# Kernel tuning notes

Hardware: AMD Instinct MI355X
Metric: run time of the kernel (lower is better)

Reference implementation:

```python
import jax, jax.numpy as jnp
import numpy as np
import math

N = 50000   # nodes
E = 800000  # edges
D = 128     # in/out dim
T = 4       # node types
H = 8       # heads (forced: Linear(8,64).view(-1, H, 8))
DK = D // H
HD = 8      # h_mat feature dim


def setup_inputs() -> dict:
    key = jax.random.key(0)
    ks = jax.random.split(key, 16)
    g = lambda k, shp, fan: jax.random.uniform(k, shp, jnp.float32, -1.0, 1.0) * math.sqrt(6.0 / fan)
    return {
        "meta_xs": jax.random.normal(ks[0], (N, D), jnp.float32),
        "node_type": jax.random.randint(ks[1], (N,), 0, T),
        "edge_index": jax.random.randint(ks[2], (2, E), 0, N),
        "h_mat": jax.random.normal(ks[3], (N, HD), jnp.float32),
        "sub_W": g(ks[4], (T, D, D), 2 * D),
        "sub_b": jnp.zeros((T, D), jnp.float32),
        "neigh_W": g(ks[5], (T, D, D), 2 * D),
        "neigh_b": jnp.zeros((T, D), jnp.float32),
        "hsub_W": g(ks[6], (HD, H * HD), HD + H * HD),
        "hsub_b": jnp.zeros((H * HD,), jnp.float32),
        "hneigh_W": g(ks[7], (HD, H * HD), HD + H * HD),
        "hneigh_b": jnp.zeros((H * HD,), jnp.float32),
        "relation_att": g(ks[8], (T, H, DK), H + DK),
        "relation_h_att": g(ks[9], (T, H, HD), H + HD),
        "ln_gamma": jnp.ones((D,), jnp.float32),
        "ln_beta": jnp.zeros((D,), jnp.float32),
    }


def _hgt_forward(meta_xs, h_mat, sub_W, sub_b, neigh_W, neigh_b, hsub_W, hsub_b,
                 hneigh_W, hneigh_b, relation_att, relation_h_att, ln_gamma, ln_beta,
                 node_type, edge_index):
    n = meta_xs.shape[0]
    e = edge_index.shape[1]
    src = edge_index[0]  # edge_index_j (neighbor)
    dst = edge_index[1]  # edge_index_i (sub / target)
    sqrt_dk = math.sqrt(DK)
    d_h = math.sqrt(H)

    # per-node, type-selected linear projections (sub by own type, neigh by own type)
    q_all = jnp.einsum('nd,tdo->tno', meta_xs, sub_W) + sub_b[:, None, :]      # [T,N,D]
    k_all = jnp.einsum('nd,tdo->tno', meta_xs, neigh_W) + neigh_b[:, None, :]  # [T,N,D]
    ar = jnp.arange(n)
    q_node = q_all[node_type, ar]  # [N,D] sub_linear[type_i](x_i)
    k_node = k_all[node_type, ar]  # [N,D] neigh_linear[type_j](x_j)

    h_sub_node = (h_mat @ hsub_W + hsub_b).reshape(n, H, HD)
    h_neigh_node = (h_mat @ hneigh_W + hneigh_b).reshape(n, H, HD)

    st = node_type[dst]  # sub type per edge selects relation params
    h_s = h_sub_node[dst]    # [E,H,8]
    h_n = h_neigh_node[src]  # [E,H,8]
    att_h = jnp.sum(jnp.tanh(h_s * h_n) * relation_h_att[st], axis=-1) / d_h  # [E,H]

    q_e = q_node[dst].reshape(e, H, DK)
    k_e = k_node[src].reshape(e, H, DK)
    att = jnp.sum(jnp.tanh(q_e * k_e) * relation_att[st], axis=-1) / sqrt_dk * att_h  # [E,H]

    # edge softmax over destination segments
    m = jax.ops.segment_max(att, dst, num_segments=n)  # [N,H]
    ea = jnp.exp(att - m[dst])
    denom = jax.ops.segment_sum(ea, dst, num_segments=n)
    alpha = ea / (denom[dst] + 1e-16)  # [E,H]

    msg = (k_e * alpha[:, :, None]).reshape(e, D)
    aggr = jax.ops.segment_sum(msg, dst, num_segments=n)  # [N,D]

    out = jax.nn.gelu(aggr, approximate=False)
    mu = jnp.mean(out, axis=-1, keepdims=True)
    var = jnp.var(out, axis=-1, keepdims=True)
    return (out - mu) * jax.lax.rsqrt(var + 1e-5) * ln_gamma + ln_beta


def reference(meta_xs, node_type, edge_index, h_mat, sub_W, sub_b, neigh_W, neigh_b,
              hsub_W, hsub_b, hneigh_W, hneigh_b, relation_att, relation_h_att,
              ln_gamma, ln_beta):
    return _hgt_forward(meta_xs, h_mat, sub_W, sub_b, neigh_W, neigh_b, hsub_W, hsub_b,
                        hneigh_W, hneigh_b, relation_att, relation_h_att, ln_gamma, ln_beta,
                        node_type, edge_index)
```

## Files before the change

kernel.cpp:

```cpp
#include <hip/hip_runtime.h>

typedef __bf16 bf16x8 __attribute__((ext_vector_type(8)));
typedef float f32x4 __attribute__((ext_vector_type(4)));

#define B_CHUNK 64
#define R_RANGE 4

__device__ __forceinline__ float exp2_fast(float x){
#if __has_builtin(__builtin_amdgcn_exp2f)
  return __builtin_amdgcn_exp2f(x);
#else
  return __expf(x * 0.69314718055994531f);
#endif
}
template<int CTRL>
__device__ __forceinline__ float dpp_add(float x){
  union { float f; int i; } a, b;
  a.f = x;
  b.i = __builtin_amdgcn_mov_dpp(a.i, CTRL, 0xF, 0xF, true);
  return x + b.f;
}
__device__ __forceinline__ float sum4(float x){
  x = dpp_add<0xB1>(x);
  x = dpp_add<0x4E>(x);
  return x;
}
__device__ __forceinline__ unsigned int cvt_pk_bf16(float lo, float hi){
  unsigned int r;
  asm("v_cvt_pk_bf16_f32 %0, %1, %2" : "=v"(r) : "v"(lo), "v"(hi));
  return r;
}
__device__ __forceinline__ unsigned short f2bf1(float f){
  return (unsigned short)cvt_pk_bf16(f, f);
}
__device__ __forceinline__ bf16x8 ld_bf8(const unsigned short* p){
  union { uint4 u; bf16x8 v; } c;
  c.u = *reinterpret_cast<const uint4*>(p);
  return c.v;
}
__device__ __forceinline__ bf16x8 ld_f32_to_bf8(const float* p){
  float4 lo = *reinterpret_cast<const float4*>(p);
  float4 hi = *reinterpret_cast<const float4*>(p + 4);
  union { unsigned int u[4]; bf16x8 v; } c;
  c.u[0] = cvt_pk_bf16(lo.x, lo.y);
  c.u[1] = cvt_pk_bf16(lo.z, lo.w);
  c.u[2] = cvt_pk_bf16(hi.x, hi.y);
  c.u[3] = cvt_pk_bf16(hi.z, hi.w);
  return c.v;
}

__global__ __launch_bounds__(256) void k_prep(const int* ntype, int* tcur, int* nbt,
                       int Npad, int N,
                       const float* subW, const float* neighW,
                       unsigned short* wts, unsigned short* wtn,
                       const int* ei, int E, unsigned short* hist,
                       int RNG, int HR, int NB, int WB){
  __shared__ unsigned int lsh[6272];
  int b = blockIdx.x;
  if (b < NB){
    int i = b*256 + threadIdx.x;
    if (i >= N) return;
    int lane = threadIdx.x & 63;
    int myt = ntype[i];
    unsigned long long below = (lane == 0) ? 0ull : ((~0ull) >> (64 - lane));
    #pragma unroll
    for (int tt = 0; tt < 4; ++tt){
      unsigned long long mask = __ballot(myt == tt);
      if (mask){
        int leader = __ffsll((long long)mask) - 1;
        int base = 0;
        if (lane == leader) base = atomicAdd(&tcur[tt], __popcll(mask));
        base = __shfl(base, leader);
        if (myt == tt){
          int pos = base + __popcll(mask & below);
          nbt[tt*Npad + pos] = i;
        }
      }
    }
  } else if (b < NB + WB){
    int i = (b - NB)*256 + threadIdx.x;
    int w = i >> 16;
    int r = i & 65535;
    int t = r >> 14;
    int rem = r & 16383;
    int o = rem >> 7;
    int kd = rem & 127;
    const float* src = w ? neighW : subW;
    unsigned short* dstp = w ? wtn : wts;
    dstp[(t << 14) + (o << 7) + kd] = f2bf1(src[(t << 14) + (kd << 7) + o]);
  } else {
    int sb = b - NB - WB;
    int cb = sb & (B_CHUNK - 1);
    int r  = sb / B_CHUNK;
    int lo = r * RNG;
    int half = RNG >> 1;
    for (int i = threadIdx.x; i < half; i += 256) lsh[i] = 0;
    __syncthreads();
    int C = (E + B_CHUNK - 1) / B_CHUNK;
    int e0 = cb * C;
    int e1 = e0 + C; if (e1 > E) e1 = E;
    for (int i = e0 + threadIdx.x; i < e1; i += 256){
      int d = ei[E + i] - lo;
      if ((unsigned)d < (unsigned)RNG)
        atomicAdd(&lsh[d >> 1], (d & 1) ? 65536u : 1u);
    }
    __syncthreads();
    unsigned int* hrow = reinterpret_cast<unsigned int*>(hist + (size_t)cb*HR + lo);
    for (int i = threadIdx.x; i < half; i += 256) hrow[i] = lsh[i];
  }
}

__global__ __launch_bounds__(256) void k_scan(unsigned short* hist, int HR,
                                              int* deg, int N){
  int d = blockIdx.x*256 + threadIdx.x;
  if (d >= N) return;
  unsigned run = 0;
  #pragma unroll 4
  for (int b = 0; b < B_CHUNK; ++b){
    unsigned short* p = hist + (size_t)b*HR + d;
    unsigned v = *p;
    *p = (unsigned short)run;
    run += v;
  }
  deg[d] = (int)run;
}

__global__ __launch_bounds__(256) void k_mix(const float* X,
      const unsigned short* wts, const unsigned short* wtn,
      const float* sub_b, const float* neigh_b,
      const int* nbt, const int* tcur, int Npad,
      float* q, char* kkc,
      const int* ei, unsigned short* bucket, int E,
      unsigned short* hist, int RNG, int HR,
      const float* h_mat, const float* hsW, const float* hsb,
      const float* hnW, const float* hnb,
      float2* hs2, char* hnc, int N, int MB, int SBL){
  __shared__ unsigned int lsh[6272];
  int b = blockIdx.x;
  if (b < MB){
    int t = -1, chunk = 0, acc = 0;
    #pragma unroll
    for (int tt = 0; tt < 4; ++tt){
      int cnt = tcur[tt];
      int nc = (cnt + 63) >> 6;
      if (t < 0 && b < acc + nc){ t = tt; chunk = b - acc; }
      acc += nc;
    }
    if (t < 0) return;
    int lane = threadIdx.x & 63;
    int w = threadIdx.x >> 6;
    int quad = lane >> 4, l16 = lane & 15;
    int cnt = tcur[t];
    int p = chunk*64 + w*16 + l16;
    bool ok = p < cnt;
    int nid = nbt[t*Npad + (ok ? p : 0)];
    bf16x8 xb[4];
    #pragma unroll
    for (int kk = 0; kk < 4; ++kk)
      xb[kk] = ld_f32_to_bf8(X + (size_t)nid*128 + kk*32 + quad*8);
    #pragma unroll
    for (int pj = 0; pj < 2; ++pj){
      const unsigned short* Wt = pj ? wtn : wts;
      const float* bias = pj ? neigh_b : sub_b;
      #pragma unroll
      for (int ot = 0; ot < 8; ++ot){
        f32x4 c = {0.f, 0.f, 0.f, 0.f};
        #pragma unroll
        for (int kk = 0; kk < 4; ++kk){
          bf16x8 wa = ld_bf8(Wt + ((size_t)t << 14) + ((size_t)(ot*16 + l16) << 7)
                                + kk*32 + quad*8);
          c = __builtin_amdgcn_mfma_f32_16x16x32_bf16(wa, xb[kk], c, 0, 0, 0);
        }
        int o0 = ot*16 + quad*4;
        float4 b4 = *reinterpret_cast<const float4*>(bias + t*128 + o0);
        if (ok){
          if (pj == 0){
            float4 v = make_float4(c[0]+b4.x, c[1]+b4.y, c[2]+b4.z, c[3]+b4.w);
            *reinterpret_cast<float4*>(q + (size_t)nid*128 + o0) = v;
          } else {
            uint2 pk;
            pk.x = cvt_pk_bf16(c[0]+b4.x, c[1]+b4.y);
            pk.y = cvt_pk_bf16(c[2]+b4.z, c[3]+b4.w);
            *reinterpret_cast<uint2*>(kkc + ((size_t)nid << 8) + (size_t)(o0 << 1)) = pk;
          }
        }
      }
    }
  } else if (b < MB + SBL){
    int sb = b - MB;
    int cb = sb & (B_CHUNK - 1);
    int r  = sb / B_CHUNK;
    int lo = r * RNG;
    int half = RNG >> 1;
    const unsigned int* hrow =
        reinterpret_cast<const unsigned int*>(hist + (size_t)cb*HR + lo);
    for (int i = threadIdx.x; i < half; i += 256) lsh[i] = hrow[i];
    __syncthreads();
    int C = (E + B_CHUNK - 1) / B_CHUNK;
    int e0 = cb * C;
    int e1 = e0 + C; if (e1 > E) e1 = E;
    for (int i = e0 + threadIdx.x; i < e1; i += 256){
      int d = ei[E + i];
      int rb = d - lo;
      if ((unsigned)rb < (unsigned)RNG){
        unsigned old = atomicAdd(&lsh[rb >> 1], (rb & 1) ? 65536u : 1u);
        unsigned pos = (old >> ((rb & 1) << 4)) & 0xffffu;
        if (pos < 128)
          bucket[(size_t)d*128 + pos] = (unsigned short)ei[i];
      }
    }
  } else {
    int i = (b - MB - SBL)*256 + threadIdx.x;
    if (i >= N*32) return;
    int n = i >> 5, l = i & 31;
    const float* hm = h_mat + (size_t)n*8;
    const float2* hsW2 = reinterpret_cast<const float2*>(hsW);
    const float2* hnW2 = reinterpret_cast<const float2*>(hnW);
    float s0=0.f, s1=0.f, n0=0.f, n1=0.f;
    #pragma unroll
    for (int d = 0; d < 8; ++d){
      float hv = hm[d];
      float2 ws2 = hsW2[d*32 + l];
      float2 wn2 = hnW2[d*32 + l];
      s0 += hv * ws2.x; s1 += hv * ws2.y;
      n0 += hv * wn2.x; n1 += hv * wn2.y;
    }
    float2 bs = reinterpret_cast<const float2*>(hsb)[l];
    float2 bn = reinterpret_cast<const float2*>(hnb)[l];
    hs2[(size_t)i] = make_float2(s0 + bs.x, s1 + bs.y);
    *reinterpret_cast<unsigned int*>(hnc + (size_t)n*128 + l*4)
        = cvt_pk_bf16(n0 + bn.x, n1 + bn.y);
  }
}

__global__ __launch_bounds__(256) void k_edge(const float* q, const char* kkc,
      const char* hnc, const float2* hs2, const int* degA,
      const unsigned short* bucket, const int* ntype,
      const float* rel_att, const float* rel_h_att,
      const float* ln_g, const float* ln_b,
      float* out, int N){
  int wid = (blockIdx.x*blockDim.x + threadIdx.x) >> 6;
  if (wid >= N) return;
  int lane = threadIdx.x & 63;
  int l = lane & 31;
  int half = (lane >> 5) & 1;
  int t4 = l & 3, head = l >> 2;
  const float TLOG2E = 2.8853900817779268f;
  float4 qv = *reinterpret_cast<const float4*>(q + (size_t)wid*128 + l*4);
  float qe0 = qv.x*TLOG2E, qe1 = qv.y*TLOG2E, qe2 = qv.z*TLOG2E, qe3 = qv.w*TLOG2E;
  float2 hv = hs2[(size_t)wid*32 + l];
  float he0 = hv.x*TLOG2E, he1 = hv.y*TLOG2E;
  int st = ntype[wid];
  int rb = st*8 + head;
  float4 ra = *reinterpret_cast<const float4*>(rel_att + rb*16 + t4*4);
  float2 rh = *reinterpret_cast<const float2*>(rel_h_att + rb*8 + t4*2);
  float c0 = -0.5f*ra.x, c1 = -0.5f*ra.y, c2 = -0.5f*ra.z, c3 = -0.5f*ra.w;
  float cs = 0.25f*(ra.x + ra.y + ra.z + ra.w);
  const float HSC = 0.35355339059327373f * 1.4426950408889634f;
  float rh0 = rh.x*HSC, rh1 = rh.y*HSC;
  float ch0 = -2.f*rh0, ch1 = -2.f*rh1, chs = rh0 + rh1;
  float s = 0.f, a0 = 0.f, a1 = 0.f, a2 = 0.f, a3 = 0.f;

  int deg = __builtin_amdgcn_readfirstlane(degA[wid]);
  if (deg > 128) deg = 128;
  unsigned bkt = reinterpret_cast<const unsigned*>(bucket)[(size_t)wid*64 + lane];
  int niter = (deg + 1) >> 1;
  const char* kk_l = kkc + l*8;
  const char* hn_l = hnc + l*4;

  struct KH { uint2 k; unsigned h; };
  auto lp = [&](int g)->KH {
    int gg = g < niter ? g : 0;
    unsigned v = (unsigned)__builtin_amdgcn_readlane((int)bkt, gg);
    int sA = (int)(v & 0xffffu);
    int sB = (2*gg + 1 < deg) ? (int)(v >> 16) : sA;
    int sy = half ? sB : sA;
    KH r;
    r.k = *reinterpret_cast<const uint2*>(kk_l + ((size_t)(unsigned)sy << 8));
    r.h = *reinterpret_cast<const unsigned*>(hn_l + ((size_t)(unsigned)sy << 7));
    return r;
  };
  auto pr = [&](KH P, int g){
    union { unsigned u; float f; } k0,k1,k2,k3,h0,h1;
    k0.u = P.k.x << 16; k1.u = P.k.x & 0xffff0000u;
    k2.u = P.k.y << 16; k3.u = P.k.y & 0xffff0000u;
    h0.u = P.h << 16;   h1.u = P.h & 0xffff0000u;
    float e0 = exp2_fast(qe0*k0.f), e1 = exp2_fast(qe1*k1.f);
    float e2 = exp2_fast(qe2*k2.f), e3 = exp2_fast(qe3*k3.f);
    float f0 = exp2_fast(he0*h0.f), f1 = exp2_fast(he1*h1.f);
    float r0 = __builtin_amdgcn_rcpf(e0 + 1.f), r1 = __builtin_amdgcn_rcpf(e1 + 1.f);
    float r2 = __builtin_amdgcn_rcpf(e2 + 1.f), r3 = __builtin_amdgcn_rcpf(e3 + 1.f);
    float g0 = __builtin_amdgcn_rcpf(f0 + 1.f), g1 = __builtin_amdgcn_rcpf(f1 + 1.f);
    float pp = fmaf(c0,r0, fmaf(c1,r1, fmaf(c2,r2, fmaf(c3,r3, cs))));
    float ph = fmaf(ch0,g0, fmaf(ch1,g1, chs));
    pp = sum4(pp);
    ph = sum4(ph);
    float w = exp2_fast(pp * ph);
    w = (2*g + half < deg) ? w : 0.f;
    s += w;
    a0 = fmaf(w, k0.f, a0); a1 = fmaf(w, k1.f, a1);
    a2 = fmaf(w, k2.f, a2); a3 = fmaf(w, k3.f, a3);
  };

  if (niter > 0){
    KH A = lp(0);
    KH B = lp(1);
    for (int g = 0; g < niter; g += 2){
      KH C = lp(g+2);
      pr(A, g);
      KH D = lp(g+3);
      if (g+1 < niter) pr(B, g+1);
      A = C; B = D;
    }
  }
  s  += __shfl_xor(s, 32);
  a0 += __shfl_xor(a0, 32); a1 += __shfl_xor(a1, 32);
  a2 += __shfl_xor(a2, 32); a3 += __shfl_xor(a3, 32);

  float inv = 1.0f / (s + 1e-16f);
  float x0 = a0*inv, x1 = a1*inv, x2 = a2*inv, x3 = a3*inv;
  const float IS2 = 0.70710678118654752f;
  x0 = 0.5f*x0*(1.f + erff(x0*IS2));
  x1 = 0.5f*x1*(1.f + erff(x1*IS2));
  x2 = 0.5f*x2*(1.f + erff(x2*IS2));
  x3 = 0.5f*x3*(1.f + erff(x3*IS2));
  float sm = x0+x1+x2+x3;
  float sq = x0*x0 + x1*x1 + x2*x2 + x3*x3;
  #pragma unroll
  for (int d = 1; d < 32; d <<= 1){ sm += __shfl_xor(sm, d); sq += __shfl_xor(sq, d); }
  float mu = sm * (1.f/128.f);
  float var = fmaxf(sq * (1.f/128.f) - mu*mu, 0.f);
  float r = rsqrtf(var + 1e-5f);
  if (half == 0){
    float4 g4 = *reinterpret_cast<const float4*>(ln_g + l*4);
    float4 b4 = *reinterpret_cast<const float4*>(ln_b + l*4);
    float4 o4 = make_float4((x0-mu)*r*g4.x + b4.x, (x1-mu)*r*g4.y + b4.y,
                            (x2-mu)*r*g4.z + b4.z, (x3-mu)*r*g4.w + b4.w);
    *reinterpret_cast<float4*>(out + (size_t)wid*128 + l*4) = o4;
  }
}

extern "C" void kernel_launch(void* const* d_in, const int* in_sizes, int n_in,
                              void* d_out, int out_size, void* d_ws, size_t ws_size,
                              hipStream_t stream) {
  const float* meta_xs  = (const float*)d_in[0];
  const int*   node_type= (const int*)d_in[1];
  const int*   edge_idx = (const int*)d_in[2];
  const float* h_mat    = (const float*)d_in[3];
  const float* sub_W    = (const float*)d_in[4];
  const float* sub_b    = (const float*)d_in[5];
  const float* neigh_W  = (const float*)d_in[6];
  const float* neigh_b  = (const float*)d_in[7];
  const float* hsub_W   = (const float*)d_in[8];
  const float* hsub_b   = (const float*)d_in[9];
  const float* hneigh_W = (const float*)d_in[10];
  const float* hneigh_b = (const float*)d_in[11];
  const float* rel_att  = (const float*)d_in[12];
  const float* rel_hatt = (const float*)d_in[13];
  const float* ln_g     = (const float*)d_in[14];
  const float* ln_b     = (const float*)d_in[15];

  const int N = in_sizes[0] / 128;
  const int E = in_sizes[2] / 2;
  const int Npad = (N + 63) & ~63;
  const int RNG = (((N + R_RANGE - 1) / R_RANGE) + 1) & ~1;
  const int HR  = RNG * R_RANGE;

  char* wbase = (char*)d_ws;
  size_t o = 0;
  auto carve = [&](size_t bytes)->char* {
    char* p = wbase + o;
    o = (o + bytes + 255) & ~(size_t)255;
    return p;
  };
  float*          q      = (float*)carve((size_t)N*128*4);
  char*           kkc    = carve((size_t)N*256);
  char*           hnc    = carve((size_t)N*128);
  float2*         hs2    = (float2*)carve((size_t)N*32*8);
  unsigned short* bucket = (unsigned short*)carve((size_t)N*128*2);
  unsigned short* hist   = (unsigned short*)carve((size_t)B_CHUNK*HR*2);
  int*            deg    = (int*)carve((size_t)N*4);
  int*            tmeta  = (int*)carve(64);
  int*            nbt    = (int*)carve((size_t)4*Npad*4);
  unsigned short* wts    = (unsigned short*)carve((size_t)4*128*128*2);
  unsigned short* wtn    = (unsigned short*)carve((size_t)4*128*128*2);
  if (o > ws_size) return;

  int* tcur = tmeta;

  const int NB  = (N + 255) / 256;
  const int WB  = (2*4*128*128) / 256;
  const int SBL = B_CHUNK * R_RANGE;
  const int MB  = ((N + 63) >> 6) + 4;
  const int HB  = (N*32 + 255) / 256;

  hipMemsetAsync(tmeta, 0, 64, stream);
  k_prep <<<NB + WB + SBL, 256, 0, stream>>>(node_type, tcur, nbt, Npad, N,
                                       sub_W, neigh_W, wts, wtn,
                                       edge_idx, E, hist, RNG, HR, NB, WB);
  k_scan <<<(N + 255)/256, 256, 0, stream>>>(hist, HR, deg, N);
  k_mix  <<<MB + SBL + HB, 256, 0, stream>>>(meta_xs, wts, wtn, sub_b, neigh_b,
                                       nbt, tcur, Npad, q, kkc,
                                       edge_idx, bucket, E, hist, RNG, HR,
                                       h_mat, hsub_W, hsub_b, hneigh_W, hneigh_b,
                                       hs2, hnc, N, MB, SBL);
  k_edge <<<(N+3)/4, 256, 0, stream>>>(q, kkc, hnc, hs2, deg, bucket, node_type,
                                       rel_att, rel_hatt, ln_g, ln_b,
                                       (float*)d_out, N);
}
```

Before: 292.5 us.

## Record per-edge ranks during histogram pass to make scatter atomic-free

The histogram pass now stores each edge's local rank within its (chunk, destination) bin. The bucket scatter then becomes a plain lookup of prefix plus rank with no shared-memory atomics, and it is split into finer per-chunk segments for more parallelism. The destination range split is halved, so each histogram block covers twice as many bins and uses more LDS, and the h_mat projections move next to the scan kernel. This adds a per-edge rank buffer write and read in exchange for removing the repeated range filtering and the second round of atomics in the scatter.

```diff
diff --git a/kernel.cpp b/kernel.cpp
--- a/kernel.cpp
+++ b/kernel.cpp
@@ -4,7 +4,7 @@
 typedef float f32x4 __attribute__((ext_vector_type(4)));
 
 #define B_CHUNK 64
-#define R_RANGE 4
+#define R_RANGE 2
 
 __device__ __forceinline__ float exp2_fast(float x){
 #if __has_builtin(__builtin_amdgcn_exp2f)
@@ -54,11 +54,32 @@
                        const float* subW, const float* neighW,
                        unsigned short* wts, unsigned short* wtn,
                        const int* ei, int E, unsigned short* hist,
-                       int RNG, int HR, int NB, int WB){
-  __shared__ unsigned int lsh[6272];
+                       unsigned short* rank, int RNG, int HR, int NB){
+  __shared__ unsigned int lsh[12544];
   int b = blockIdx.x;
-  if (b < NB){
-    int i = b*256 + threadIdx.x;
+  const int SB1 = B_CHUNK * R_RANGE;
+  if (b < SB1){
+    int cb = b & (B_CHUNK - 1);
+    int r  = b >> 6;
+    int lo = r * RNG;
+    int bins = RNG >> 1;
+    for (int i = threadIdx.x; i < bins; i += 256) lsh[i] = 0;
+    __syncthreads();
+    int C = (E + B_CHUNK - 1) / B_CHUNK;
+    int e0 = cb * C;
+    int e1 = e0 + C; if (e1 > E) e1 = E;
+    for (int i = e0 + threadIdx.x; i < e1; i += 256){
+      int d = ei[E + i] - lo;
+      if ((unsigned)d < (unsigned)RNG){
+        unsigned old = atomicAdd(&lsh[d >> 1], (d & 1) ? 65536u : 1u);
+        rank[i] = (unsigned short)((old >> ((d & 1) << 4)) & 0xffffu);
+      }
+    }
+    __syncthreads();
+    unsigned int* hrow = reinterpret_cast<unsigned int*>(hist + (size_t)cb*HR + lo);
+    for (int i = threadIdx.x; i < bins; i += 256) hrow[i] = lsh[i];
+  } else if (b < SB1 + NB){
+    int i = (b - SB1)*256 + threadIdx.x;
     if (i >= N) return;
     int lane = threadIdx.x & 63;
     int myt = ntype[i];
@@ -77,8 +98,8 @@
         }
       }
     }
-  } else if (b < NB + WB){
-    int i = (b - NB)*256 + threadIdx.x;
+  } else {
+    int i = (b - SB1 - NB)*256 + threadIdx.x;
     int w = i >> 16;
     int r = i & 65535;
     int t = r >> 14;
@@ -88,54 +109,58 @@
     const float* src = w ? neighW : subW;
     unsigned short* dstp = w ? wtn : wts;
     dstp[(t << 14) + (o << 7) + kd] = f2bf1(src[(t << 14) + (kd << 7) + o]);
+  }
+}
+
+__global__ __launch_bounds__(256) void k_mid(unsigned short* hist, int HR,
+                       int* deg, int N, int SCB,
+                       const float* h_mat, const float* hsW, const float* hsb,
+                       const float* hnW, const float* hnb,
+                       float2* hs2, char* hnc){
+  int b = blockIdx.x;
+  if (b < SCB){
+    int d = b*256 + threadIdx.x;
+    if (d >= N) return;
+    unsigned run = 0;
+    #pragma unroll 4
+    for (int c = 0; c < B_CHUNK; ++c){
+      unsigned short* p = hist + (size_t)c*HR + d;
+      unsigned v = *p;
+      *p = (unsigned short)run;
+      run += v;
+    }
+    deg[d] = (int)run;
   } else {
-    int sb = b - NB - WB;
-    int cb = sb & (B_CHUNK - 1);
-    int r  = sb / B_CHUNK;
-    int lo = r * RNG;
-    int half = RNG >> 1;
-    for (int i = threadIdx.x; i < half; i += 256) lsh[i] = 0;
-    __syncthreads();
-    int C = (E + B_CHUNK - 1) / B_CHUNK;
-    int e0 = cb * C;
-    int e1 = e0 + C; if (e1 > E) e1 = E;
-    for (int i = e0 + threadIdx.x; i < e1; i += 256){
-      int d = ei[E + i] - lo;
-      if ((unsigned)d < (unsigned)RNG)
-        atomicAdd(&lsh[d >> 1], (d & 1) ? 65536u : 1u);
-    }
-    __syncthreads();
-    unsigned int* hrow = reinterpret_cast<unsigned int*>(hist + (size_t)cb*HR + lo);
-    for (int i = threadIdx.x; i < half; i += 256) hrow[i] = lsh[i];
+    int i = (b - SCB)*256 + threadIdx.x;
+    if (i >= N*32) return;
+    int n = i >> 5, l = i & 31;
+    const float* hm = h_mat + (size_t)n*8;
+    const float2* hsW2 = reinterpret_cast<const float2*>(hsW);
+    const float2* hnW2 = reinterpret_cast<const float2*>(hnW);
+    float s0=0.f, s1=0.f, n0=0.f, n1=0.f;
+    #pragma unroll
+    for (int d = 0; d < 8; ++d){
+      float hv = hm[d];
+      float2 ws2 = hsW2[d*32 + l];
+      float2 wn2 = hnW2[d*32 + l];
+      s0 += hv * ws2.x; s1 += hv * ws2.y;
+      n0 += hv * wn2.x; n1 += hv * wn2.y;
+    }
+    float2 bs = reinterpret_cast<const float2*>(hsb)[l];
+    float2 bn = reinterpret_cast<const float2*>(hnb)[l];
+    hs2[(size_t)i] = make_float2(s0 + bs.x, s1 + bs.y);
+    *reinterpret_cast<unsigned int*>(hnc + (size_t)n*128 + l*4)
+        = cvt_pk_bf16(n0 + bn.x, n1 + bn.y);
   }
 }
 
-__global__ __launch_bounds__(256) void k_scan(unsigned short* hist, int HR,
-                                              int* deg, int N){
-  int d = blockIdx.x*256 + threadIdx.x;
-  if (d >= N) return;
-  unsigned run = 0;
-  #pragma unroll 4
-  for (int b = 0; b < B_CHUNK; ++b){
-    unsigned short* p = hist + (size_t)b*HR + d;
-    unsigned v = *p;
-    *p = (unsigned short)run;
-    run += v;
-  }
-  deg[d] = (int)run;
-}
-
-__global__ __launch_bounds__(256) void k_mix(const float* X,
+__global__ __launch_bounds__(256) void k_ms(const float* X,
       const unsigned short* wts, const unsigned short* wtn,
       const float* sub_b, const float* neigh_b,
       const int* nbt, const int* tcur, int Npad,
       float* q, char* kkc,
       const int* ei, unsigned short* bucket, int E,
-      unsigned short* hist, int RNG, int HR,
-      const float* h_mat, const float* hsW, const float* hsb,
-      const float* hnW, const float* hnb,
-      float2* hs2, char* hnc, int N, int MB, int SBL){
-  __shared__ unsigned int lsh[6272];
+      const unsigned short* hist, int HR, const unsigned short* rank, int MB){
   int b = blockIdx.x;
   if (b < MB){
     int t = -1, chunk = 0, acc = 0;
@@ -186,50 +211,22 @@
         }
       }
     }
-  } else if (b < MB + SBL){
+  } else {
     int sb = b - MB;
-    int cb = sb & (B_CHUNK - 1);
-    int r  = sb / B_CHUNK;
-    int lo = r * RNG;
-    int half = RNG >> 1;
-    const unsigned int* hrow =
-        reinterpret_cast<const unsigned int*>(hist + (size_t)cb*HR + lo);
-    for (int i = threadIdx.x; i < half; i += 256) lsh[i] = hrow[i];
-    __syncthreads();
+    int cb = sb >> 3;
+    int sub = sb & 7;
     int C = (E + B_CHUNK - 1) / B_CHUNK;
-    int e0 = cb * C;
-    int e1 = e0 + C; if (e1 > E) e1 = E;
+    int seg = (C + 7) >> 3;
+    int s0 = sub*seg;
+    int s1 = s0 + seg; if (s1 > C) s1 = C;
+    int e0 = cb*C + s0;
+    int e1 = cb*C + s1; if (e1 > E) e1 = E;
+    const unsigned short* hrow = hist + (size_t)cb*HR;
     for (int i = e0 + threadIdx.x; i < e1; i += 256){
       int d = ei[E + i];
-      int rb = d - lo;
-      if ((unsigned)rb < (unsigned)RNG){
-        unsigned old = atomicAdd(&lsh[rb >> 1], (rb & 1) ? 65536u : 1u);
-        unsigned pos = (old >> ((rb & 1) << 4)) & 0xffffu;
-        if (pos < 128)
-          bucket[(size_t)d*128 + pos] = (unsigned short)ei[i];
-      }
-    }
-  } else {
-    int i = (b - MB - SBL)*256 + threadIdx.x;
-    if (i >= N*32) return;
-    int n = i >> 5, l = i & 31;
-    const float* hm = h_mat + (size_t)n*8;
-    const float2* hsW2 = reinterpret_cast<const float2*>(hsW);
-    const float2* hnW2 = reinterpret_cast<const float2*>(hnW);
-    float s0=0.f, s1=0.f, n0=0.f, n1=0.f;
-    #pragma unroll
-    for (int d = 0; d < 8; ++d){
-      float hv = hm[d];
-      float2 ws2 = hsW2[d*32 + l];
-      float2 wn2 = hnW2[d*32 + l];
-      s0 += hv * ws2.x; s1 += hv * ws2.y;
-      n0 += hv * wn2.x; n1 += hv * wn2.y;
-    }
-    float2 bs = reinterpret_cast<const float2*>(hsb)[l];
-    float2 bn = reinterpret_cast<const float2*>(hnb)[l];
-    hs2[(size_t)i] = make_float2(s0 + bs.x, s1 + bs.y);
-    *reinterpret_cast<unsigned int*>(hnc + (size_t)n*128 + l*4)
-        = cvt_pk_bf16(n0 + bn.x, n1 + bn.y);
+      int pos = (int)hrow[d] + (int)rank[i];
+      if (pos < 128) bucket[(size_t)d*128 + pos] = (unsigned short)ei[i];
+    }
   }
 }
 
@@ -379,6 +376,7 @@
   float2*         hs2    = (float2*)carve((size_t)N*32*8);
   unsigned short* bucket = (unsigned short*)carve((size_t)N*128*2);
   unsigned short* hist   = (unsigned short*)carve((size_t)B_CHUNK*HR*2);
+  unsigned short* rank   = (unsigned short*)carve((size_t)E*2);
   int*            deg    = (int*)carve((size_t)N*4);
   int*            tmeta  = (int*)carve(64);
   int*            nbt    = (int*)carve((size_t)4*Npad*4);
@@ -388,22 +386,24 @@
 
   int* tcur = tmeta;
 
+  const int SB1 = B_CHUNK * R_RANGE;
   const int NB  = (N + 255) / 256;
   const int WB  = (2*4*128*128) / 256;
-  const int SBL = B_CHUNK * R_RANGE;
+  const int SCB = (N + 255) / 256;
+  const int HB  = (N*32 + 255) / 256;
   const int MB  = ((N + 63) >> 6) + 4;
-  const int HB  = (N*32 + 255) / 256;
+  const int SB3 = B_CHUNK * 8;
 
   hipMemsetAsync(tmeta, 0, 64, stream);
-  k_prep <<<NB + WB + SBL, 256, 0, stream>>>(node_type, tcur, nbt, Npad, N,
+  k_prep <<<SB1 + NB + WB, 256, 0, stream>>>(node_type, tcur, nbt, Npad, N,
                                        sub_W, neigh_W, wts, wtn,
-                                       edge_idx, E, hist, RNG, HR, NB, WB);
-  k_scan <<<(N + 255)/256, 256, 0, stream>>>(hist, HR, deg, N);
-  k_mix  <<<MB + SBL + HB, 256, 0, stream>>>(meta_xs, wts, wtn, sub_b, neigh_b,
+                                       edge_idx, E, hist, rank, RNG, HR, NB);
+  k_mid  <<<SCB + HB, 256, 0, stream>>>(hist, HR, deg, N, SCB,
+                                       h_mat, hsub_W, hsub_b, hneigh_W, hneigh_b,
+                                       hs2, hnc);
+  k_ms   <<<MB + SB3, 256, 0, stream>>>(meta_xs, wts, wtn, sub_b, neigh_b,
                                        nbt, tcur, Npad, q, kkc,
-                                       edge_idx, bucket, E, hist, RNG, HR,
-                                       h_mat, hsub_W, hsub_b, hneigh_W, hneigh_b,
-                                       hs2, hnc, N, MB, SBL);
+                                       edge_idx, bucket, E, hist, HR, rank, MB);
   k_edge <<<(N+3)/4, 256, 0, stream>>>(q, kkc, hnc, hs2, deg, bucket, node_type,
                                        rel_att, rel_hatt, ln_g, ln_b,
                                        (float*)d_out, N);
```

Result: no change. 291.8 us (-0.2%).
